# Optimization experiments

Hardware: AMD Instinct MI355X
Metric: run time of the kernel (lower is better)

The kernel has to match this reference:

```python
import jax, jax.numpy as jnp
import numpy as np

N_AB = 1024
N = 2049  # odd; alpha[N//2] == pi/2
H = 64


def setup_inputs() -> dict:
    key = jax.random.key(0)
    k0, k1, k2, k3, k4, k5 = jax.random.split(key, 6)
    alpha = jnp.linspace(0.0, jnp.pi, N).astype(jnp.float32)
    s = 0.3  # keep tanh in its active range
    w0 = jax.random.normal(k0, (N_AB, H, 1), jnp.float32) * s
    w1 = jax.random.normal(k1, (N_AB, H, H), jnp.float32) * s
    w2 = jax.random.normal(k2, (N_AB, 2, H), jnp.float32) * s
    b0 = jax.random.normal(k3, (N_AB, H), jnp.float32) * s
    b1 = jax.random.normal(k4, (N_AB, H), jnp.float32) * s
    # original init: last bias = sqrt(ab_initial) with ab_initial > 0
    b2 = jnp.sqrt(jax.random.uniform(k5, (N_AB, 2), jnp.float32, 0.5, 2.0))
    return dict(alpha=alpha, w0=w0, w1=w1, w2=w2, b0=b0, b1=b1, b2=b2)


def _mlp(x, w0, w1, w2, b0, b1, b2):
    # x: (N_ab, B, 1) -> (N_ab, B, 2); squared output as in the torch module
    h = jnp.tanh(jnp.einsum('Nij,NBj->NBi', w0, x) + b0[:, None, :])
    h = jnp.tanh(jnp.einsum('Nij,NBj->NBi', w1, h) + b1[:, None, :])
    out = jnp.einsum('Nij,NBj->NBi', w2, h) + b2[:, None, :]
    return out * out


def reference(alpha, w0, w1, w2, b0, b1, b2):
    n = alpha.shape[0]
    half = n // 2 + 1
    n_ab = w0.shape[0]
    ah = alpha[:half]                                   # (B,)
    x_in = jnp.broadcast_to(ah[None, :, None], (n_ab, half, 1))
    # torch's double-backward trick == forward-mode derivative wrt a uniform
    # scalar shift of the input, i.e. a single JVP with tangent ones.
    f = lambda x: _mlp(x, w0, w1, w2, b0, b1, b2)
    x, dab = jax.jvp(f, (x_in,), (jnp.ones_like(x_in),))
    a, b = x[..., 0], x[..., 1]
    da, db = dab[..., 0], dab[..., 1]
    ca = jnp.cos(ah)[None, :]
    sa = jnp.sin(ah)[None, :]
    xp = a * (ca - 1.0)
    yp = b * sa
    xpp = -a * sa + da * (ca - 1.0)
    ypp = b * ca + db * sa
    flip = lambda t: t[:, :-1][:, ::-1]                 # mirror without midpoint
    xp = jnp.concatenate([xp, 2.0 * xp[:, -1:] - flip(xp)], axis=1)
    yp = jnp.concatenate([yp, flip(yp)], axis=1)
    xpp = jnp.concatenate([xpp, flip(xpp)], axis=1)
    ypp = jnp.concatenate([ypp, -flip(ypp)], axis=1)
    return xp, yp, xpp, ypp
```

## Files before the change

kernel.cpp:

```cpp
#include <hip/hip_runtime.h>

#define N_AB  1024
#define NHALF 1025
#define NFULL 2049
#define HDIM  64
#define PLANE ((size_t)N_AB * NFULL)
#define C2L   2.8853900817779268f

typedef __bf16 bf16x8 __attribute__((ext_vector_type(8)));
typedef __bf16 bf16x4 __attribute__((ext_vector_type(4)));
typedef float  f32x4  __attribute__((ext_vector_type(4)));
typedef float  f32x2  __attribute__((ext_vector_type(2)));

#define MFMA16(A,B,C) __builtin_amdgcn_mfma_f32_16x16x32_bf16(A,B,C,0,0,0)

#define TBL2(IX2,H2,O2) { \
    float _f0 = __builtin_amdgcn_fmed3f(IX2.x, 0.5f, 2047.0f); \
    float _f1 = __builtin_amdgcn_fmed3f(IX2.y, 0.5f, 2047.0f); \
    f32x2 _e0 = s_tanh2[(int)_f0]; \
    f32x2 _e1 = s_tanh2[(int)_f1]; \
    H2.x = _e0.x; H2.y = _e1.x; \
    O2.x = _e0.y; O2.y = _e1.y; }

#define L1P(I0, WI2, BI2, WD2, BV, BT) { \
    f32x2 _ix = __builtin_elementwise_fma(WI2, x2, BI2); \
    f32x2 _h, _o; TBL2(_ix,_h,_o) \
    f32x2 _bt = _o * WD2; \
    BV[I0] = (__bf16)_h.x; BV[I0+1] = (__bf16)_h.y; \
    BT[I0] = (__bf16)_bt.x; BT[I0+1] = (__bf16)_bt.y; }

#define L2P(AVI2, AT2, FV, FT, I0) { \
    f32x2 _h, _o; TBL2(AVI2,_h,_o) \
    f32x2 _dh = _o * (AT2); \
    FV[I0] = (__bf16)_h.x;  FV[I0+1] = (__bf16)_h.y; \
    FT[I0] = (__bf16)_dh.x; FT[I0+1] = (__bf16)_dh.y; }

#define COMPUTE_TILE(P) \
    const f32x4 tg = s_trig[P]; \
    const float sa = tg.y, cam1 = tg.z, ca = tg.w; \
    const f32x2 x2 = {tg.x, tg.x}; \
    bf16x8 bv0, bv1, bt0, bt1; \
    L1P(0, w0iA.xy, b0iA.xy, w0dA.xy, bv0, bt0) \
    L1P(2, w0iA.zw, b0iA.zw, w0dA.zw, bv0, bt0) \
    L1P(4, w0iB.xy, b0iB.xy, w0dB.xy, bv0, bt0) \
    L1P(6, w0iB.zw, b0iB.zw, w0dB.zw, bv0, bt0) \
    L1P(0, w0iC.xy, b0iC.xy, w0dC.xy, bv1, bt1) \
    L1P(2, w0iC.zw, b0iC.zw, w0dC.zw, bv1, bt1) \
    L1P(4, w0iD.xy, b0iD.xy, w0dD.xy, bv1, bt1) \
    L1P(6, w0iD.zw, b0iD.zw, w0dD.zw, bv1, bt1) \
    const f32x4 zz = {0.0f,0.0f,0.0f,0.0f}; \
    f32x4 av0 = MFMA16(A01,bv1,MFMA16(A00,bv0,b1i0)); \
    f32x4 av1 = MFMA16(A11,bv1,MFMA16(A10,bv0,b1i1)); \
    f32x4 av2 = MFMA16(A21,bv1,MFMA16(A20,bv0,b1i2)); \
    f32x4 av3 = MFMA16(A31,bv1,MFMA16(A30,bv0,b1i3)); \
    f32x4 at0 = MFMA16(A01,bt1,MFMA16(A00,bt0,zz)); \
    f32x4 at1 = MFMA16(A11,bt1,MFMA16(A10,bt0,zz)); \
    f32x4 at2 = MFMA16(A21,bt1,MFMA16(A20,bt0,zz)); \
    f32x4 at3 = MFMA16(A31,bt1,MFMA16(A30,bt0,zz)); \
    bf16x8 hv0, hv1, ht0, ht1; \
    L2P(av0.xy, at0.xy, hv0, ht0, 0) \
    L2P(av0.zw, at0.zw, hv0, ht0, 2) \
    L2P(av1.xy, at1.xy, hv0, ht0, 4) \
    L2P(av1.zw, at1.zw, hv0, ht0, 6) \
    L2P(av2.xy, at2.xy, hv1, ht1, 0) \
    L2P(av2.zw, at2.zw, hv1, ht1, 2) \
    L2P(av3.xy, at3.xy, hv1, ht1, 4) \
    L2P(av3.zw, at3.zw, hv1, ht1, 6) \
    f32x4 pvq = MFMA16(W2F1, hv1, MFMA16(W2F0, hv0, c2f)); \
    f32x4 ptq = MFMA16(W2F1, ht1, MFMA16(W2F0, ht0, zz)); \
    const float z0  = __shfl(pvq[0], col); \
    const float z1  = __shfl(pvq[1], col); \
    const float pt0 = __shfl(ptq[0], col); \
    const float pt1 = __shfl(ptq[1], col); \
    const float aa = z0*z0, bb = z1*z1; \
    const float da = 2.0f*z0*pt0, db = 2.0f*z1*pt1; \
    const float xp = aa*cam1, yp = bb*sa; \
    const float xpp = fmaf(da,cam1,-(aa*sa)); \
    const float ypp = fmaf(bb,ca, db*sa);

__global__ void __launch_bounds__(256, 2) sofa_kernel(
    const float* __restrict__ alpha,
    const float* __restrict__ w0,
    const float* __restrict__ w1,
    const float* __restrict__ w2,
    const float* __restrict__ b0,
    const float* __restrict__ b1,
    const float* __restrict__ b2,
    float* __restrict__ out)
{
    __shared__ __align__(16) __bf16 w1s[HDIM * HDIM];
    __shared__ __align__(16) f32x4 s_trig[NHALF];
    __shared__ __align__(16) f32x2 s_tanh2[2048];
    __shared__ float s_xplast;

    const int n    = blockIdx.x;
    const int tid  = threadIdx.x;
    const int lane = tid & 63;
    const int wid  = tid >> 6;
    const int col  = lane & 15;
    const int grp  = lane >> 4;

    const float* __restrict__ w0n = w0 + (size_t)n * HDIM;
    const float* __restrict__ b0n = b0 + (size_t)n * HDIM;
    const float* __restrict__ w1n = w1 + (size_t)n * HDIM * HDIM;
    const float* __restrict__ b1n = b1 + (size_t)n * HDIM;
    const float* __restrict__ w2n = w2 + (size_t)n * 2 * HDIM;
    const float* __restrict__ b2n = b2 + (size_t)n * 2;

    for (int e = tid; e < NHALF; e += 256) {
        const float xx = alpha[e];
        const float cc = __cosf(xx);
        f32x4 t; t.x = xx; t.y = __sinf(xx); t.z = cc - 1.0f; t.w = cc;
        s_trig[e] = t;
    }
    for (int e = tid; e < 2048; e += 256) {
        const float z = (float)(e - 1024) * 0.00390625f;
        const float ee = __builtin_amdgcn_exp2f(z * C2L);
        const float th = fmaf(-2.0f, __builtin_amdgcn_rcpf(1.0f + ee), 1.0f);
        f32x2 en; en.x = th; en.y = fmaf(-th, th, 1.0f);
        s_tanh2[e] = en;
    }
    for (int e4 = tid; e4 < (HDIM * HDIM) / 4; e4 += 256) {
        const int i = e4 >> 4, j4 = (e4 & 15) << 2;
        f32x4 v = ((const f32x4*)w1n)[e4];
        bf16x4 b;
        b[0] = (__bf16)(v.x * 256.0f); b[1] = (__bf16)(v.y * 256.0f);
        b[2] = (__bf16)(v.z * 256.0f); b[3] = (__bf16)(v.w * 256.0f);
        *(bf16x4*)&w1s[i * 64 + (((j4 >> 3) ^ (i & 7)) << 3) + (j4 & 7)] = b;
    }
    __syncthreads();

    const int jb0 = grp * 8, jb1 = 32 + grp * 8;
    f32x4 w0iA = *(const f32x4*)(w0n + jb0);
    f32x4 w0iB = *(const f32x4*)(w0n + jb0 + 4);
    f32x4 w0iC = *(const f32x4*)(w0n + jb1);
    f32x4 w0iD = *(const f32x4*)(w0n + jb1 + 4);
    const f32x4 w0dA = w0iA * 0.00390625f;
    const f32x4 w0dB = w0iB * 0.00390625f;
    const f32x4 w0dC = w0iC * 0.00390625f;
    const f32x4 w0dD = w0iD * 0.00390625f;
    w0iA *= 256.0f; w0iB *= 256.0f; w0iC *= 256.0f; w0iD *= 256.0f;
    f32x4 b0iA = *(const f32x4*)(b0n + jb0);
    f32x4 b0iB = *(const f32x4*)(b0n + jb0 + 4);
    f32x4 b0iC = *(const f32x4*)(b0n + jb1);
    f32x4 b0iD = *(const f32x4*)(b0n + jb1 + 4);
    b0iA = b0iA * 256.0f + 1024.5f; b0iB = b0iB * 256.0f + 1024.5f;
    b0iC = b0iC * 256.0f + 1024.5f; b0iD = b0iD * 256.0f + 1024.5f;

    f32x4 b1i0 = *(const f32x4*)(b1n + 0  + grp * 4);
    f32x4 b1i1 = *(const f32x4*)(b1n + 16 + grp * 4);
    f32x4 b1i2 = *(const f32x4*)(b1n + 32 + grp * 4);
    f32x4 b1i3 = *(const f32x4*)(b1n + 48 + grp * 4);
    b1i0 = b1i0 * 256.0f + 1024.5f; b1i1 = b1i1 * 256.0f + 1024.5f;
    b1i2 = b1i2 * 256.0f + 1024.5f; b1i3 = b1i3 * 256.0f + 1024.5f;

    const float* __restrict__ w2row = w2n + (col < 2 ? col * HDIM : 0);
    f32x4 qa = *(const f32x4*)(w2row + grp * 4);
    f32x4 qb = *(const f32x4*)(w2row + 16 + grp * 4);
    f32x4 qc = *(const f32x4*)(w2row + 32 + grp * 4);
    f32x4 qd = *(const f32x4*)(w2row + 48 + grp * 4);
    if (col >= 2) {
        qa = (f32x4){0.0f,0.0f,0.0f,0.0f}; qb = qa; qc = qa; qd = qa;
    }
    bf16x8 W2F0, W2F1;
    W2F0[0]=(__bf16)qa.x; W2F0[1]=(__bf16)qa.y; W2F0[2]=(__bf16)qa.z; W2F0[3]=(__bf16)qa.w;
    W2F0[4]=(__bf16)qb.x; W2F0[5]=(__bf16)qb.y; W2F0[6]=(__bf16)qb.z; W2F0[7]=(__bf16)qb.w;
    W2F1[0]=(__bf16)qc.x; W2F1[1]=(__bf16)qc.y; W2F1[2]=(__bf16)qc.z; W2F1[3]=(__bf16)qc.w;
    W2F1[4]=(__bf16)qd.x; W2F1[5]=(__bf16)qd.y; W2F1[6]=(__bf16)qd.z; W2F1[7]=(__bf16)qd.w;

    f32x4 c2f = {0.0f, 0.0f, 0.0f, 0.0f};
    if (grp == 0) { c2f[0] = b2n[0]; c2f[1] = b2n[1]; }

    const bf16x8* w1v = (const bf16x8*)w1s;
    const int sw = col & 7;
#define AF(RT,KH) w1v[((RT)*16 + col)*8 + (((KH)*4 + grp) ^ sw)]
    const bf16x8 A00 = AF(0,0), A01 = AF(0,1), A10 = AF(1,0), A11 = AF(1,1);
    const bf16x8 A20 = AF(2,0), A21 = AF(2,1), A30 = AF(3,0), A31 = AF(3,1);

    const size_t obase = (size_t)grp * PLANE + (size_t)n * NFULL;

    if (wid == 0) {
        COMPUTE_TILE(1024)
        if (col == 0) {
            out[obase + 1024] = (grp == 0) ? xp : (grp == 1) ? yp : (grp == 2) ? xpp : ypp;
            if (grp == 0) s_xplast = xp;
        }
    }
    __syncthreads();
    const float xl2 = 2.0f * s_xplast;

    #pragma unroll 1
    for (int it = 0; it < 16; ++it) {
        const int p = ((it * 4 + wid) << 4) + col;
        COMPUTE_TILE(p)
        const float vdir = (grp == 0) ? xp : (grp == 1) ? yp : (grp == 2) ? xpp : ypp;
        const float vmir = (grp == 0) ? (xl2 - xp)
                         : (grp == 1) ? yp
                         : (grp == 2) ? xpp : -ypp;
        out[obase + p] = vdir;
        out[obase + (2048 - p)] = vmir;
    }
}

extern "C" void kernel_launch(void* const* d_in, const int* in_sizes, int n_in,
                              void* d_out, int out_size, void* d_ws, size_t ws_size,
                              hipStream_t stream) {
    const float* alpha = (const float*)d_in[0];
    const float* w0    = (const float*)d_in[1];
    const float* w1    = (const float*)d_in[2];
    const float* w2    = (const float*)d_in[3];
    const float* b0    = (const float*)d_in[4];
    const float* b1    = (const float*)d_in[5];
    const float* b2    = (const float*)d_in[6];
    float* out = (float*)d_out;
    sofa_kernel<<<dim3(N_AB), dim3(256), 0, stream>>>(alpha, w0, w1, w2, b0, b1, b2, out);
}
```

Baseline: 48.42 us.

## Pack tanh table as bf16 pairs and fold w0 into tangent weight matrix

Stores the tanh and 1−tanh² values as a packed bf16 pair in one 32-bit LDS word, and builds layer-1 bf16 operands with byte permutes instead of per-element conversions. The layer-0 tangent scaling by w0 moves into a second pre-scaled copy of w1 kept in LDS and registers, so the per-point derivative multiply goes away. Each lane now computes only its own output plane via selects, which simplifies the epilogue and mirror write. This costs more LDS and extra register fragments, and lowers derivative precision because 1−tanh² is stored in bf16.

```diff
diff --git a/kernel.cpp b/kernel.cpp
--- a/kernel.cpp
+++ b/kernel.cpp
@@ -11,72 +11,85 @@
 typedef __bf16 bf16x4 __attribute__((ext_vector_type(4)));
 typedef float  f32x4  __attribute__((ext_vector_type(4)));
 typedef float  f32x2  __attribute__((ext_vector_type(2)));
+typedef unsigned int u32;
+typedef u32    u32x4  __attribute__((ext_vector_type(4)));
 
 #define MFMA16(A,B,C) __builtin_amdgcn_mfma_f32_16x16x32_bf16(A,B,C,0,0,0)
-
-#define TBL2(IX2,H2,O2) { \
-    float _f0 = __builtin_amdgcn_fmed3f(IX2.x, 0.5f, 2047.0f); \
-    float _f1 = __builtin_amdgcn_fmed3f(IX2.y, 0.5f, 2047.0f); \
-    f32x2 _e0 = s_tanh2[(int)_f0]; \
-    f32x2 _e1 = s_tanh2[(int)_f1]; \
-    H2.x = _e0.x; H2.y = _e1.x; \
-    O2.x = _e0.y; O2.y = _e1.y; }
-
-#define L1P(I0, WI2, BI2, WD2, BV, BT) { \
+#define MED3(F) __builtin_amdgcn_fmed3f((F), 0.5f, 2047.0f)
+
+#define L1P(W, WI2, BI2, BVW, BTW) { \
     f32x2 _ix = __builtin_elementwise_fma(WI2, x2, BI2); \
-    f32x2 _h, _o; TBL2(_ix,_h,_o) \
-    f32x2 _bt = _o * WD2; \
-    BV[I0] = (__bf16)_h.x; BV[I0+1] = (__bf16)_h.y; \
-    BT[I0] = (__bf16)_bt.x; BT[I0+1] = (__bf16)_bt.y; }
-
-#define L2P(AVI2, AT2, FV, FT, I0) { \
-    f32x2 _h, _o; TBL2(AVI2,_h,_o) \
+    u32 _e0 = s_tbl[(int)MED3(_ix.x)]; \
+    u32 _e1 = s_tbl[(int)MED3(_ix.y)]; \
+    BVW[W] = __builtin_amdgcn_perm(_e1, _e0, 0x05040100u); \
+    BTW[W] = __builtin_amdgcn_perm(_e1, _e0, 0x07060302u); }
+
+#define L2P(AVI2, AT2, HVW, FT, I0) { \
+    u32 _e0 = s_tbl[(int)MED3(AVI2.x)]; \
+    u32 _e1 = s_tbl[(int)MED3(AVI2.y)]; \
+    HVW[(I0)>>1] = __builtin_amdgcn_perm(_e1, _e0, 0x05040100u); \
+    f32x2 _o; \
+    _o.x = __builtin_bit_cast(float, _e0 & 0xFFFF0000u); \
+    _o.y = __builtin_bit_cast(float, _e1 & 0xFFFF0000u); \
     f32x2 _dh = _o * (AT2); \
-    FV[I0] = (__bf16)_h.x;  FV[I0+1] = (__bf16)_h.y; \
     FT[I0] = (__bf16)_dh.x; FT[I0+1] = (__bf16)_dh.y; }
 
 #define COMPUTE_TILE(P) \
     const f32x4 tg = s_trig[P]; \
     const float sa = tg.y, cam1 = tg.z, ca = tg.w; \
     const f32x2 x2 = {tg.x, tg.x}; \
-    bf16x8 bv0, bv1, bt0, bt1; \
-    L1P(0, w0iA.xy, b0iA.xy, w0dA.xy, bv0, bt0) \
-    L1P(2, w0iA.zw, b0iA.zw, w0dA.zw, bv0, bt0) \
-    L1P(4, w0iB.xy, b0iB.xy, w0dB.xy, bv0, bt0) \
-    L1P(6, w0iB.zw, b0iB.zw, w0dB.zw, bv0, bt0) \
-    L1P(0, w0iC.xy, b0iC.xy, w0dC.xy, bv1, bt1) \
-    L1P(2, w0iC.zw, b0iC.zw, w0dC.zw, bv1, bt1) \
-    L1P(4, w0iD.xy, b0iD.xy, w0dD.xy, bv1, bt1) \
-    L1P(6, w0iD.zw, b0iD.zw, w0dD.zw, bv1, bt1) \
+    u32x4 bvw0, bvw1, btw0, btw1; \
+    L1P(0, w0iA.xy, b0iA.xy, bvw0, btw0) \
+    L1P(1, w0iA.zw, b0iA.zw, bvw0, btw0) \
+    L1P(2, w0iB.xy, b0iB.xy, bvw0, btw0) \
+    L1P(3, w0iB.zw, b0iB.zw, bvw0, btw0) \
+    L1P(0, w0iC.xy, b0iC.xy, bvw1, btw1) \
+    L1P(1, w0iC.zw, b0iC.zw, bvw1, btw1) \
+    L1P(2, w0iD.xy, b0iD.xy, bvw1, btw1) \
+    L1P(3, w0iD.zw, b0iD.zw, bvw1, btw1) \
+    const bf16x8 bv0 = __builtin_bit_cast(bf16x8, bvw0); \
+    const bf16x8 bv1 = __builtin_bit_cast(bf16x8, bvw1); \
+    const bf16x8 bt0 = __builtin_bit_cast(bf16x8, btw0); \
+    const bf16x8 bt1 = __builtin_bit_cast(bf16x8, btw1); \
     const f32x4 zz = {0.0f,0.0f,0.0f,0.0f}; \
     f32x4 av0 = MFMA16(A01,bv1,MFMA16(A00,bv0,b1i0)); \
     f32x4 av1 = MFMA16(A11,bv1,MFMA16(A10,bv0,b1i1)); \
     f32x4 av2 = MFMA16(A21,bv1,MFMA16(A20,bv0,b1i2)); \
     f32x4 av3 = MFMA16(A31,bv1,MFMA16(A30,bv0,b1i3)); \
-    f32x4 at0 = MFMA16(A01,bt1,MFMA16(A00,bt0,zz)); \
-    f32x4 at1 = MFMA16(A11,bt1,MFMA16(A10,bt0,zz)); \
-    f32x4 at2 = MFMA16(A21,bt1,MFMA16(A20,bt0,zz)); \
-    f32x4 at3 = MFMA16(A31,bt1,MFMA16(A30,bt0,zz)); \
-    bf16x8 hv0, hv1, ht0, ht1; \
-    L2P(av0.xy, at0.xy, hv0, ht0, 0) \
-    L2P(av0.zw, at0.zw, hv0, ht0, 2) \
-    L2P(av1.xy, at1.xy, hv0, ht0, 4) \
-    L2P(av1.zw, at1.zw, hv0, ht0, 6) \
-    L2P(av2.xy, at2.xy, hv1, ht1, 0) \
-    L2P(av2.zw, at2.zw, hv1, ht1, 2) \
-    L2P(av3.xy, at3.xy, hv1, ht1, 4) \
-    L2P(av3.zw, at3.zw, hv1, ht1, 6) \
+    f32x4 at0 = MFMA16(T01,bt1,MFMA16(T00,bt0,zz)); \
+    f32x4 at1 = MFMA16(T11,bt1,MFMA16(T10,bt0,zz)); \
+    f32x4 at2 = MFMA16(T21,bt1,MFMA16(T20,bt0,zz)); \
+    f32x4 at3 = MFMA16(T31,bt1,MFMA16(T30,bt0,zz)); \
+    u32x4 hvw0_; bf16x8 ht0, ht1; \
+    u32x4 hvw1_; \
+    L2P(av0.xy, at0.xy, hvw0_, ht0, 0) \
+    L2P(av0.zw, at0.zw, hvw0_, ht0, 2) \
+    L2P(av1.xy, at1.xy, hvw0_, ht0, 4) \
+    L2P(av1.zw, at1.zw, hvw0_, ht0, 6) \
+    L2P(av2.xy, at2.xy, hvw1_, ht1, 0) \
+    L2P(av2.zw, at2.zw, hvw1_, ht1, 2) \
+    L2P(av3.xy, at3.xy, hvw1_, ht1, 4) \
+    L2P(av3.zw, at3.zw, hvw1_, ht1, 6) \
+    const bf16x8 hv0 = __builtin_bit_cast(bf16x8, hvw0_); \
+    const bf16x8 hv1 = __builtin_bit_cast(bf16x8, hvw1_); \
     f32x4 pvq = MFMA16(W2F1, hv1, MFMA16(W2F0, hv0, c2f)); \
     f32x4 ptq = MFMA16(W2F1, ht1, MFMA16(W2F0, ht0, zz)); \
-    const float z0  = __shfl(pvq[0], col); \
-    const float z1  = __shfl(pvq[1], col); \
-    const float pt0 = __shfl(ptq[0], col); \
-    const float pt1 = __shfl(ptq[1], col); \
-    const float aa = z0*z0, bb = z1*z1; \
-    const float da = 2.0f*z0*pt0, db = 2.0f*z1*pt1; \
-    const float xp = aa*cam1, yp = bb*sa; \
-    const float xpp = fmaf(da,cam1,-(aa*sa)); \
-    const float ypp = fmaf(bb,ca, db*sa);
+     \
+    const float z0s  = __shfl(pvq[0], col); \
+    const float z1s  = __shfl(pvq[1], col); \
+    const float pt0s = __shfl(ptq[0], col); \
+    const float pt1s = __shfl(ptq[1], col); \
+    const float zsel  = (grp & 1) ? z1s  : z0s; \
+    const float ptsel = (grp & 1) ? pt1s : pt0s; \
+    const float u = zsel * zsel; \
+    const float v = zsel * ptsel; \
+    const float vv = v + v; \
+    const float c01 = (grp & 1) ? sa : cam1; \
+    const float nsa = -sa; \
+    const float c23 = (grp & 1) ? ca : nsa; \
+    const float c1  = (grp & 2) ? c23 : c01; \
+    const float c2  = (grp & 2) ? c01 : 0.0f; \
+    const float pout = fmaf(u, c1, vv * c2);
 
 __global__ void __launch_bounds__(256, 2) sofa_kernel(
     const float* __restrict__ alpha,
@@ -89,8 +102,9 @@
     float* __restrict__ out)
 {
     __shared__ __align__(16) __bf16 w1s[HDIM * HDIM];
+    __shared__ __align__(16) __bf16 w1t[HDIM * HDIM];
     __shared__ __align__(16) f32x4 s_trig[NHALF];
-    __shared__ __align__(16) f32x2 s_tanh2[2048];
+    __shared__ __align__(16) u32  s_tbl[2048];
     __shared__ float s_xplast;
 
     const int n    = blockIdx.x;
@@ -117,42 +131,40 @@
         const float z = (float)(e - 1024) * 0.00390625f;
         const float ee = __builtin_amdgcn_exp2f(z * C2L);
         const float th = fmaf(-2.0f, __builtin_amdgcn_rcpf(1.0f + ee), 1.0f);
-        f32x2 en; en.x = th; en.y = fmaf(-th, th, 1.0f);
-        s_tanh2[e] = en;
+        const float om = fmaf(-th, th, 1.0f);
+        const u32 hu = (u32)__builtin_bit_cast(unsigned short, (__bf16)th);
+        const u32 ou = (u32)__builtin_bit_cast(unsigned short, (__bf16)om);
+        s_tbl[e] = (ou << 16) | hu;
     }
     for (int e4 = tid; e4 < (HDIM * HDIM) / 4; e4 += 256) {
         const int i = e4 >> 4, j4 = (e4 & 15) << 2;
-        f32x4 v = ((const f32x4*)w1n)[e4];
-        bf16x4 b;
-        b[0] = (__bf16)(v.x * 256.0f); b[1] = (__bf16)(v.y * 256.0f);
-        b[2] = (__bf16)(v.z * 256.0f); b[3] = (__bf16)(v.w * 256.0f);
-        *(bf16x4*)&w1s[i * 64 + (((j4 >> 3) ^ (i & 7)) << 3) + (j4 & 7)] = b;
+        const f32x4 v  = ((const f32x4*)w1n)[e4];
+        const f32x4 wv = ((const f32x4*)w0n)[e4 & 15];
+        bf16x4 bv, bt;
+        bv[0] = (__bf16)(v.x * 256.0f); bv[1] = (__bf16)(v.y * 256.0f);
+        bv[2] = (__bf16)(v.z * 256.0f); bv[3] = (__bf16)(v.w * 256.0f);
+        bt[0] = (__bf16)(v.x * wv.x);   bt[1] = (__bf16)(v.y * wv.y);
+        bt[2] = (__bf16)(v.z * wv.z);   bt[3] = (__bf16)(v.w * wv.w);
+        const int adr = i * 64 + (((j4 >> 3) ^ (i & 7)) << 3) + (j4 & 7);
+        *(bf16x4*)&w1s[adr] = bv;
+        *(bf16x4*)&w1t[adr] = bt;
     }
     __syncthreads();
 
     const int jb0 = grp * 8, jb1 = 32 + grp * 8;
-    f32x4 w0iA = *(const f32x4*)(w0n + jb0);
-    f32x4 w0iB = *(const f32x4*)(w0n + jb0 + 4);
-    f32x4 w0iC = *(const f32x4*)(w0n + jb1);
-    f32x4 w0iD = *(const f32x4*)(w0n + jb1 + 4);
-    const f32x4 w0dA = w0iA * 0.00390625f;
-    const f32x4 w0dB = w0iB * 0.00390625f;
-    const f32x4 w0dC = w0iC * 0.00390625f;
-    const f32x4 w0dD = w0iD * 0.00390625f;
-    w0iA *= 256.0f; w0iB *= 256.0f; w0iC *= 256.0f; w0iD *= 256.0f;
-    f32x4 b0iA = *(const f32x4*)(b0n + jb0);
-    f32x4 b0iB = *(const f32x4*)(b0n + jb0 + 4);
-    f32x4 b0iC = *(const f32x4*)(b0n + jb1);
-    f32x4 b0iD = *(const f32x4*)(b0n + jb1 + 4);
-    b0iA = b0iA * 256.0f + 1024.5f; b0iB = b0iB * 256.0f + 1024.5f;
-    b0iC = b0iC * 256.0f + 1024.5f; b0iD = b0iD * 256.0f + 1024.5f;
-
-    f32x4 b1i0 = *(const f32x4*)(b1n + 0  + grp * 4);
-    f32x4 b1i1 = *(const f32x4*)(b1n + 16 + grp * 4);
-    f32x4 b1i2 = *(const f32x4*)(b1n + 32 + grp * 4);
-    f32x4 b1i3 = *(const f32x4*)(b1n + 48 + grp * 4);
-    b1i0 = b1i0 * 256.0f + 1024.5f; b1i1 = b1i1 * 256.0f + 1024.5f;
-    b1i2 = b1i2 * 256.0f + 1024.5f; b1i3 = b1i3 * 256.0f + 1024.5f;
+    f32x4 w0iA = *(const f32x4*)(w0n + jb0) * 256.0f;
+    f32x4 w0iB = *(const f32x4*)(w0n + jb0 + 4) * 256.0f;
+    f32x4 w0iC = *(const f32x4*)(w0n + jb1) * 256.0f;
+    f32x4 w0iD = *(const f32x4*)(w0n + jb1 + 4) * 256.0f;
+    f32x4 b0iA = *(const f32x4*)(b0n + jb0) * 256.0f + 1024.5f;
+    f32x4 b0iB = *(const f32x4*)(b0n + jb0 + 4) * 256.0f + 1024.5f;
+    f32x4 b0iC = *(const f32x4*)(b0n + jb1) * 256.0f + 1024.5f;
+    f32x4 b0iD = *(const f32x4*)(b0n + jb1 + 4) * 256.0f + 1024.5f;
+
+    f32x4 b1i0 = *(const f32x4*)(b1n + 0  + grp * 4) * 256.0f + 1024.5f;
+    f32x4 b1i1 = *(const f32x4*)(b1n + 16 + grp * 4) * 256.0f + 1024.5f;
+    f32x4 b1i2 = *(const f32x4*)(b1n + 32 + grp * 4) * 256.0f + 1024.5f;
+    f32x4 b1i3 = *(const f32x4*)(b1n + 48 + grp * 4) * 256.0f + 1024.5f;
 
     const float* __restrict__ w2row = w2n + (col < 2 ? col * HDIM : 0);
     f32x4 qa = *(const f32x4*)(w2row + grp * 4);
@@ -172,33 +184,35 @@
     if (grp == 0) { c2f[0] = b2n[0]; c2f[1] = b2n[1]; }
 
     const bf16x8* w1v = (const bf16x8*)w1s;
+    const bf16x8* w1tv = (const bf16x8*)w1t;
     const int sw = col & 7;
-#define AF(RT,KH) w1v[((RT)*16 + col)*8 + (((KH)*4 + grp) ^ sw)]
-    const bf16x8 A00 = AF(0,0), A01 = AF(0,1), A10 = AF(1,0), A11 = AF(1,1);
-    const bf16x8 A20 = AF(2,0), A21 = AF(2,1), A30 = AF(3,0), A31 = AF(3,1);
+#define AF(SRC,RT,KH) SRC[((RT)*16 + col)*8 + (((KH)*4 + grp) ^ sw)]
+    const bf16x8 A00 = AF(w1v,0,0), A01 = AF(w1v,0,1), A10 = AF(w1v,1,0), A11 = AF(w1v,1,1);
+    const bf16x8 A20 = AF(w1v,2,0), A21 = AF(w1v,2,1), A30 = AF(w1v,3,0), A31 = AF(w1v,3,1);
+    const bf16x8 T00 = AF(w1tv,0,0), T01 = AF(w1tv,0,1), T10 = AF(w1tv,1,0), T11 = AF(w1tv,1,1);
+    const bf16x8 T20 = AF(w1tv,2,0), T21 = AF(w1tv,2,1), T30 = AF(w1tv,3,0), T31 = AF(w1tv,3,1);
 
     const size_t obase = (size_t)grp * PLANE + (size_t)n * NFULL;
 
     if (wid == 0) {
         COMPUTE_TILE(1024)
         if (col == 0) {
-            out[obase + 1024] = (grp == 0) ? xp : (grp == 1) ? yp : (grp == 2) ? xpp : ypp;
-            if (grp == 0) s_xplast = xp;
+            out[obase + 1024] = pout;
+            if (grp == 0) s_xplast = pout;
         }
     }
     __syncthreads();
+
     const float xl2 = 2.0f * s_xplast;
+    const float s_mir = ((grp ^ (grp >> 1)) & 1) ? 1.0f : -1.0f;
+    const float a_mir = (grp == 0) ? xl2 : 0.0f;
 
     #pragma unroll 1
     for (int it = 0; it < 16; ++it) {
         const int p = ((it * 4 + wid) << 4) + col;
         COMPUTE_TILE(p)
-        const float vdir = (grp == 0) ? xp : (grp == 1) ? yp : (grp == 2) ? xpp : ypp;
-        const float vmir = (grp == 0) ? (xl2 - xp)
-                         : (grp == 1) ? yp
-                         : (grp == 2) ? xpp : -ypp;
-        out[obase + p] = vdir;
-        out[obase + (2048 - p)] = vmir;
+        out[obase + p] = pout;
+        out[obase + (2048 - p)] = fmaf(pout, s_mir, a_mir);
     }
 }
 
```

Measured after the change: 46.71 us. 1.04x faster.
